# Optimization experiments

Hardware: AMD Instinct MI355X
Metric: run time of the kernel (lower is better)

Reference implementation:

```python
import jax, jax.numpy as jnp
import numpy as np

B, S, D_IN, D_OUT, RANK, HBS, ABS = 4, 2048, 4096, 4096, 32, 128, 16


def _hadamard(n: int) -> np.ndarray:
    H = np.array([[1.0]], dtype=np.float64)
    while H.shape[0] < n:
        H = np.block([[H, H], [H, -H]])
    return (H / np.sqrt(n)).astype(np.float32)


def setup_inputs() -> dict:
    key = jax.random.key(0)
    ks = jax.random.split(key, 6)
    x = jax.random.normal(ks[0], (B, S, D_IN), dtype=jnp.float32)
    # random +/-1 sign vector (matches torch.randint(0,2)*2-1)
    S_in = (jax.random.randint(ks[1], (D_IN,), 0, 2) * 2 - 1).astype(jnp.float32)
    H_block = jnp.asarray(_hadamard(HBS))  # orthonormal block Hadamard
    w_quantized = jax.random.normal(ks[2], (D_OUT, D_IN), dtype=jnp.float32) * 0.02
    lora_a = jax.random.normal(ks[3], (RANK, D_IN), dtype=jnp.float32) * 0.01
    lora_b = jax.random.normal(ks[4], (D_OUT, RANK), dtype=jnp.float32) * 0.01
    bias = jax.random.normal(ks[5], (D_OUT,), dtype=jnp.float32) * 0.01
    return {"x": x, "S_in": S_in, "H_block": H_block, "w_quantized": w_quantized,
            "lora_a": lora_a, "lora_b": lora_b, "bias": bias}


def _quantize_nvfp4(x, block_size=ABS):
    # per-block (size 16) NVFP4 fake-quant; numel here is divisible by block_size
    levels = jnp.array([0.0, 0.5, 1.0, 1.5, 2.0, 3.0, 4.0, 6.0], dtype=x.dtype)
    shape = x.shape
    xf = x.reshape(-1, block_size)
    amax = jnp.maximum(jnp.max(jnp.abs(xf), axis=-1, keepdims=True), 1e-12)
    scale = amax / 6.0
    x_norm = jnp.abs(xf) / scale
    idx = jnp.argmin(jnp.abs(x_norm[..., None] - levels), axis=-1)  # snap to grid
    xq = jnp.sign(xf) * levels[idx] * scale
    return xq.reshape(shape)


def _hadamard_rotate(x, S_in, H_block):
    # sign flip then block-diagonal Hadamard on the last dim
    shape = x.shape
    x_s = x * S_in
    x3 = x_s.reshape(*shape[:-1], shape[-1] // HBS, HBS)
    return (x3 @ H_block).reshape(shape)


def reference(x, S_in, H_block, w_quantized, lora_a, lora_b, bias):
    x_rot = _hadamard_rotate(x, S_in, H_block)          # [B,S,D_IN]
    x_q = _quantize_nvfp4(x_rot)                        # NVFP4 fake-quant activations
    out = jnp.einsum('bsd,od->bso', x_q, w_quantized)   # main GEMM
    # LoRA correction on the (unquantized) rotated activations
    out = out + jnp.einsum('bsr,or->bso', jnp.einsum('bsd,rd->bsr', x_rot, lora_a), lora_b)
    out = out + bias
    return out
```

## Files before the change

### kernel.cpp

```cpp
#include <hip/hip_runtime.h>

#define M_ROWS 8192
#define DIN    4096
#define DOUT   4096
#define RANK   32
#define KAUG   4128

typedef __attribute__((ext_vector_type(8))) short short8;
typedef __attribute__((ext_vector_type(4))) float floatx4;

__device__ __forceinline__ unsigned short f2bf(float f) {
    unsigned int u = __float_as_uint(f);
    unsigned int r = (u + 0x7FFFu + ((u >> 16) & 1u)) >> 16;
    return (unsigned short)r;
}

__global__ __launch_bounds__(256) void rot_quant_kernel(
    const float* __restrict__ x, const float* __restrict__ sgn,
    const float* __restrict__ lora_a, unsigned short* __restrict__ xaug)
{
    __shared__ float xs[4096];
    __shared__ float tred[RANK][9];

    const int row = blockIdx.x;
    const int t = threadIdx.x;
    const float* xr = x + (size_t)row * DIN;

    #pragma unroll
    for (int it = 0; it < 4; ++it) {
        int i4 = it * 256 + t;
        float4 v = ((const float4*)xr)[i4];
        float4 s = ((const float4*)sgn)[i4];
        v.x *= s.x; v.y *= s.y; v.z *= s.z; v.w *= s.w;
        ((float4*)xs)[i4] = v;
    }
    __syncthreads();

    for (int h = 1; h < 128; h <<= 1) {
        #pragma unroll
        for (int p = t; p < 2048; p += 256) {
            int i = ((p & ~(h - 1)) << 1) | (p & (h - 1));
            float a = xs[i], b = xs[i + h];
            xs[i] = a + b;
            xs[i + h] = a - b;
        }
        __syncthreads();
    }

    const float inv = 0.08838834764831845f;

    {
        float v[16];
        float amax = 0.f;
        #pragma unroll
        for (int j = 0; j < 16; ++j) {
            v[j] = xs[16 * t + j] * inv;
            amax = fmaxf(amax, fabsf(v[j]));
        }
        amax = fmaxf(amax, 1e-12f);
        float scale = amax / 6.0f;
        unsigned int pk[8];
        #pragma unroll
        for (int j = 0; j < 8; ++j) {
            unsigned short q2[2];
            #pragma unroll
            for (int e = 0; e < 2; ++e) {
                float vv = v[2 * j + e];
                float an = fabsf(vv) / scale;
                float lev = 0.0f;
                lev = an > 0.25f ? 0.5f : lev;
                lev = an > 0.75f ? 1.0f : lev;
                lev = an > 1.25f ? 1.5f : lev;
                lev = an > 1.75f ? 2.0f : lev;
                lev = an > 2.5f  ? 3.0f : lev;
                lev = an > 3.5f  ? 4.0f : lev;
                lev = an > 5.0f  ? 6.0f : lev;
                q2[e] = f2bf(copysignf(lev * scale, vv));
            }
            pk[j] = (unsigned int)q2[0] | ((unsigned int)q2[1] << 16);
        }
        unsigned short* orow = xaug + (size_t)row * KAUG + 16 * t;
        uint4 pk0 = make_uint4(pk[0], pk[1], pk[2], pk[3]);
        uint4 pk1 = make_uint4(pk[4], pk[5], pk[6], pk[7]);
        ((uint4*)orow)[0] = pk0;
        ((uint4*)orow)[1] = pk1;
    }

    {
        int r = t >> 3, oct = t & 7;
        const float* ar = lora_a + (size_t)r * DIN;
        float sum = 0.f;
        for (int d0 = oct * 4; d0 < DIN; d0 += 32) {
            float4 a4 = *(const float4*)(ar + d0);
            float4 x4 = *(const float4*)(xs + d0);
            sum += a4.x * x4.x + a4.y * x4.y + a4.z * x4.z + a4.w * x4.w;
        }
        tred[r][oct] = sum;
    }
    __syncthreads();
    if (t < RANK) {
        float s = 0.f;
        #pragma unroll
        for (int k = 0; k < 8; ++k) s += tred[t][k];
        s *= inv;
        xaug[(size_t)row * KAUG + DIN + t] = f2bf(s);
    }
}

__global__ __launch_bounds__(256) void cast_w_kernel(
    const float* __restrict__ w, const float* __restrict__ lora_b,
    unsigned short* __restrict__ waug)
{
    const int n = blockIdx.x;
    unsigned short* wr = waug + (size_t)n * KAUG;
    const float* wsrc = w + (size_t)n * DIN;
    #pragma unroll
    for (int j = threadIdx.x; j < DIN; j += 256) wr[j] = f2bf(wsrc[j]);
    if (threadIdx.x < RANK)
        wr[DIN + threadIdx.x] = f2bf(lora_b[(size_t)n * RANK + threadIdx.x]);
}

__global__ __launch_bounds__(256) void gemm_kernel(
    const unsigned short* __restrict__ A,
    const unsigned short* __restrict__ Bm,
    const float* __restrict__ bias,
    float* __restrict__ C)
{
    __shared__ unsigned short As[128 * 32];
    __shared__ unsigned short Bs[128 * 32];

    const int nt = blockIdx.x & 31;
    const int mt = blockIdx.x >> 5;
    const int m0 = mt * 128, n0 = nt * 128;
    const int t = threadIdx.x;
    const int wave = t >> 6, lane = t & 63;
    const int wm = wave & 1, wn = wave >> 1;
    const int lm = lane & 15, lq = lane >> 4;

    floatx4 acc[4][4] = {};

    for (int kk = 0; kk < KAUG; kk += 32) {
        __syncthreads();
        {
            const int c0 = wave * 2;
            const int r_ = (c0 << 4) + (lane >> 2);
            const int colb = (lane & 3) << 3;
            const unsigned short* ga = A + (size_t)(m0 + r_) * KAUG + kk + colb;
            __builtin_amdgcn_global_load_lds(
                (const __attribute__((address_space(1))) void*)ga,
                (__attribute__((address_space(3))) void*)(As + (c0 << 9)), 16, 0, 0);
            __builtin_amdgcn_global_load_lds(
                (const __attribute__((address_space(1))) void*)(ga + (size_t)16 * KAUG),
                (__attribute__((address_space(3))) void*)(As + ((c0 + 1) << 9)), 16, 0, 0);
            const unsigned short* gb = Bm + (size_t)(n0 + r_) * KAUG + kk + colb;
            __builtin_amdgcn_global_load_lds(
                (const __attribute__((address_space(1))) void*)gb,
                (__attribute__((address_space(3))) void*)(Bs + (c0 << 9)), 16, 0, 0);
            __builtin_amdgcn_global_load_lds(
                (const __attribute__((address_space(1))) void*)(gb + (size_t)16 * KAUG),
                (__attribute__((address_space(3))) void*)(Bs + ((c0 + 1) << 9)), 16, 0, 0);
        }
        __syncthreads();

        short8 af[4], bfr[4];
        #pragma unroll
        for (int mi = 0; mi < 4; ++mi)
            af[mi] = *(const short8*)&As[(wm * 64 + mi * 16 + lm) * 32 + lq * 8];
        #pragma unroll
        for (int ni = 0; ni < 4; ++ni)
            bfr[ni] = *(const short8*)&Bs[(wn * 64 + ni * 16 + lm) * 32 + lq * 8];
        #pragma unroll
        for (int mi = 0; mi < 4; ++mi)
            #pragma unroll
            for (int ni = 0; ni < 4; ++ni)
                acc[mi][ni] = __builtin_amdgcn_mfma_f32_16x16x32_bf16(
                    af[mi], bfr[ni], acc[mi][ni], 0, 0, 0);
    }

    float bv[4];
    #pragma unroll
    for (int ni = 0; ni < 4; ++ni)
        bv[ni] = bias[n0 + wn * 64 + ni * 16 + lm];
    #pragma unroll
    for (int mi = 0; mi < 4; ++mi) {
        #pragma unroll
        for (int ni = 0; ni < 4; ++ni) {
            const int col = n0 + wn * 64 + ni * 16 + lm;
            #pragma unroll
            for (int r = 0; r < 4; ++r) {
                const int rowm = m0 + wm * 64 + mi * 16 + lq * 4 + r;
                C[(size_t)rowm * DOUT + col] = acc[mi][ni][r] + bv[ni];
            }
        }
    }
}

extern "C" void kernel_launch(void* const* d_in, const int* in_sizes, int n_in,
                              void* d_out, int out_size, void* d_ws, size_t ws_size,
                              hipStream_t stream) {
    const float* x      = (const float*)d_in[0];
    const float* sgn    = (const float*)d_in[1];
    const float* w      = (const float*)d_in[3];
    const float* lora_a = (const float*)d_in[4];
    const float* lora_b = (const float*)d_in[5];
    const float* bias   = (const float*)d_in[6];
    float* out = (float*)d_out;

    unsigned short* xaug = (unsigned short*)d_ws;
    unsigned short* waug = xaug + (size_t)M_ROWS * KAUG;

    rot_quant_kernel<<<M_ROWS, 256, 0, stream>>>(x, sgn, lora_a, xaug);
    cast_w_kernel<<<DOUT, 256, 0, stream>>>(w, lora_b, waug);
    gemm_kernel<<<(M_ROWS / 128) * (DOUT / 128), 256, 0, stream>>>(xaug, waug, bias, out);
}
```

Baseline: 781.9 us.

## Swizzle GEMM LDS tiles, batch rows in rot_quant, vectorize weight cast

Applies an XOR swizzle to the LDS column placement of the A/B tiles in the GEMM so that the MFMA fragment reads hit fewer LDS bank conflicts. The rotate/quantize kernel now handles four rows per block, reusing each lora_a load across four rows, and replaces the LDS reduction with wavefront shuffles. The weight cast uses float4 loads and packed 16-byte stores. The 64KB LDS per block in rot_quant may reduce its occupancy.

```diff
diff --git a/kernel.cpp b/kernel.cpp
--- a/kernel.cpp
+++ b/kernel.cpp
@@ -5,6 +5,7 @@
 #define DOUT   4096
 #define RANK   32
 #define KAUG   4128
+#define RROWS  4
 
 typedef __attribute__((ext_vector_type(8))) short short8;
 typedef __attribute__((ext_vector_type(4))) float floatx4;
@@ -19,42 +20,45 @@
     const float* __restrict__ x, const float* __restrict__ sgn,
     const float* __restrict__ lora_a, unsigned short* __restrict__ xaug)
 {
-    __shared__ float xs[4096];
-    __shared__ float tred[RANK][9];
-
-    const int row = blockIdx.x;
+    __shared__ float xs[RROWS][4096];
+
+    const int row0 = blockIdx.x * RROWS;
     const int t = threadIdx.x;
-    const float* xr = x + (size_t)row * DIN;
 
     #pragma unroll
     for (int it = 0; it < 4; ++it) {
         int i4 = it * 256 + t;
-        float4 v = ((const float4*)xr)[i4];
         float4 s = ((const float4*)sgn)[i4];
-        v.x *= s.x; v.y *= s.y; v.z *= s.z; v.w *= s.w;
-        ((float4*)xs)[i4] = v;
+        #pragma unroll
+        for (int r = 0; r < RROWS; ++r) {
+            float4 v = ((const float4*)(x + (size_t)(row0 + r) * DIN))[i4];
+            v.x *= s.x; v.y *= s.y; v.z *= s.z; v.w *= s.w;
+            ((float4*)xs[r])[i4] = v;
+        }
     }
     __syncthreads();
 
     for (int h = 1; h < 128; h <<= 1) {
         #pragma unroll
-        for (int p = t; p < 2048; p += 256) {
-            int i = ((p & ~(h - 1)) << 1) | (p & (h - 1));
-            float a = xs[i], b = xs[i + h];
-            xs[i] = a + b;
-            xs[i + h] = a - b;
+        for (int p = t; p < 2048 * RROWS; p += 256) {
+            int r = p >> 11, q = p & 2047;
+            int i = ((q & ~(h - 1)) << 1) | (q & (h - 1));
+            float a = xs[r][i], b = xs[r][i + h];
+            xs[r][i] = a + b;
+            xs[r][i + h] = a - b;
         }
         __syncthreads();
     }
 
     const float inv = 0.08838834764831845f;
 
-    {
+    #pragma unroll
+    for (int r = 0; r < RROWS; ++r) {
         float v[16];
         float amax = 0.f;
         #pragma unroll
         for (int j = 0; j < 16; ++j) {
-            v[j] = xs[16 * t + j] * inv;
+            v[j] = xs[r][16 * t + j] * inv;
             amax = fmaxf(amax, fabsf(v[j]));
         }
         amax = fmaxf(amax, 1e-12f);
@@ -79,31 +83,39 @@
             }
             pk[j] = (unsigned int)q2[0] | ((unsigned int)q2[1] << 16);
         }
-        unsigned short* orow = xaug + (size_t)row * KAUG + 16 * t;
-        uint4 pk0 = make_uint4(pk[0], pk[1], pk[2], pk[3]);
-        uint4 pk1 = make_uint4(pk[4], pk[5], pk[6], pk[7]);
-        ((uint4*)orow)[0] = pk0;
-        ((uint4*)orow)[1] = pk1;
+        unsigned short* orow = xaug + (size_t)(row0 + r) * KAUG + 16 * t;
+        ((uint4*)orow)[0] = make_uint4(pk[0], pk[1], pk[2], pk[3]);
+        ((uint4*)orow)[1] = make_uint4(pk[4], pk[5], pk[6], pk[7]);
     }
 
     {
-        int r = t >> 3, oct = t & 7;
-        const float* ar = lora_a + (size_t)r * DIN;
-        float sum = 0.f;
+        int rk = t >> 3, oct = t & 7;
+        const float* ar = lora_a + (size_t)rk * DIN;
+        float s0 = 0.f, s1 = 0.f, s2 = 0.f, s3 = 0.f;
         for (int d0 = oct * 4; d0 < DIN; d0 += 32) {
             float4 a4 = *(const float4*)(ar + d0);
-            float4 x4 = *(const float4*)(xs + d0);
-            sum += a4.x * x4.x + a4.y * x4.y + a4.z * x4.z + a4.w * x4.w;
-        }
-        tred[r][oct] = sum;
-    }
-    __syncthreads();
-    if (t < RANK) {
-        float s = 0.f;
-        #pragma unroll
-        for (int k = 0; k < 8; ++k) s += tred[t][k];
-        s *= inv;
-        xaug[(size_t)row * KAUG + DIN + t] = f2bf(s);
+            float4 x0 = *(const float4*)(&xs[0][d0]);
+            float4 x1 = *(const float4*)(&xs[1][d0]);
+            float4 x2 = *(const float4*)(&xs[2][d0]);
+            float4 x3 = *(const float4*)(&xs[3][d0]);
+            s0 += a4.x * x0.x + a4.y * x0.y + a4.z * x0.z + a4.w * x0.w;
+            s1 += a4.x * x1.x + a4.y * x1.y + a4.z * x1.z + a4.w * x1.w;
+            s2 += a4.x * x2.x + a4.y * x2.y + a4.z * x2.z + a4.w * x2.w;
+            s3 += a4.x * x3.x + a4.y * x3.y + a4.z * x3.z + a4.w * x3.w;
+        }
+        #pragma unroll
+        for (int m = 1; m < 8; m <<= 1) {
+            s0 += __shfl_xor(s0, m, 64);
+            s1 += __shfl_xor(s1, m, 64);
+            s2 += __shfl_xor(s2, m, 64);
+            s3 += __shfl_xor(s3, m, 64);
+        }
+        if (oct == 0) {
+            xaug[(size_t)(row0 + 0) * KAUG + DIN + rk] = f2bf(s0 * inv);
+            xaug[(size_t)(row0 + 1) * KAUG + DIN + rk] = f2bf(s1 * inv);
+            xaug[(size_t)(row0 + 2) * KAUG + DIN + rk] = f2bf(s2 * inv);
+            xaug[(size_t)(row0 + 3) * KAUG + DIN + rk] = f2bf(s3 * inv);
+        }
     }
 }
 
@@ -112,12 +124,26 @@
     unsigned short* __restrict__ waug)
 {
     const int n = blockIdx.x;
+    const int t = threadIdx.x;
     unsigned short* wr = waug + (size_t)n * KAUG;
-    const float* wsrc = w + (size_t)n * DIN;
-    #pragma unroll
-    for (int j = threadIdx.x; j < DIN; j += 256) wr[j] = f2bf(wsrc[j]);
-    if (threadIdx.x < RANK)
-        wr[DIN + threadIdx.x] = f2bf(lora_b[(size_t)n * RANK + threadIdx.x]);
+    const float* wsrc = w + (size_t)n * DIN + 16 * t;
+    float4 f0 = ((const float4*)wsrc)[0];
+    float4 f1 = ((const float4*)wsrc)[1];
+    float4 f2 = ((const float4*)wsrc)[2];
+    float4 f3 = ((const float4*)wsrc)[3];
+    uint4 p0, p1;
+    p0.x = (unsigned int)f2bf(f0.x) | ((unsigned int)f2bf(f0.y) << 16);
+    p0.y = (unsigned int)f2bf(f0.z) | ((unsigned int)f2bf(f0.w) << 16);
+    p0.z = (unsigned int)f2bf(f1.x) | ((unsigned int)f2bf(f1.y) << 16);
+    p0.w = (unsigned int)f2bf(f1.z) | ((unsigned int)f2bf(f1.w) << 16);
+    p1.x = (unsigned int)f2bf(f2.x) | ((unsigned int)f2bf(f2.y) << 16);
+    p1.y = (unsigned int)f2bf(f2.z) | ((unsigned int)f2bf(f2.w) << 16);
+    p1.z = (unsigned int)f2bf(f3.x) | ((unsigned int)f2bf(f3.y) << 16);
+    p1.w = (unsigned int)f2bf(f3.z) | ((unsigned int)f2bf(f3.w) << 16);
+    ((uint4*)(wr + 16 * t))[0] = p0;
+    ((uint4*)(wr + 16 * t))[1] = p1;
+    if (t < RANK)
+        wr[DIN + t] = f2bf(lora_b[(size_t)n * RANK + t]);
 }
 
 __global__ __launch_bounds__(256) void gemm_kernel(
@@ -136,15 +162,17 @@
     const int wave = t >> 6, lane = t & 63;
     const int wm = wave & 1, wn = wave >> 1;
     const int lm = lane & 15, lq = lane >> 4;
+    const int sw = ((lm >> 1) & 3);
 
     floatx4 acc[4][4] = {};
+
+    const int c0 = wave * 2;
+    const int r_ = (c0 << 4) + (lane >> 2);
+    const int colb = ((lane & 3) ^ ((lane >> 3) & 3)) << 3;
 
     for (int kk = 0; kk < KAUG; kk += 32) {
         __syncthreads();
         {
-            const int c0 = wave * 2;
-            const int r_ = (c0 << 4) + (lane >> 2);
-            const int colb = (lane & 3) << 3;
             const unsigned short* ga = A + (size_t)(m0 + r_) * KAUG + kk + colb;
             __builtin_amdgcn_global_load_lds(
                 (const __attribute__((address_space(1))) void*)ga,
@@ -165,10 +193,10 @@
         short8 af[4], bfr[4];
         #pragma unroll
         for (int mi = 0; mi < 4; ++mi)
-            af[mi] = *(const short8*)&As[(wm * 64 + mi * 16 + lm) * 32 + lq * 8];
+            af[mi] = *(const short8*)&As[(wm * 64 + mi * 16 + lm) * 32 + ((lq ^ sw) << 3)];
         #pragma unroll
         for (int ni = 0; ni < 4; ++ni)
-            bfr[ni] = *(const short8*)&Bs[(wn * 64 + ni * 16 + lm) * 32 + lq * 8];
+            bfr[ni] = *(const short8*)&Bs[(wn * 64 + ni * 16 + lm) * 32 + ((lq ^ sw) << 3)];
         #pragma unroll
         for (int mi = 0; mi < 4; ++mi)
             #pragma unroll
@@ -209,7 +237,7 @@
     unsigned short* xaug = (unsigned short*)d_ws;
     unsigned short* waug = xaug + (size_t)M_ROWS * KAUG;
 
-    rot_quant_kernel<<<M_ROWS, 256, 0, stream>>>(x, sgn, lora_a, xaug);
+    rot_quant_kernel<<<M_ROWS / RROWS, 256, 0, stream>>>(x, sgn, lora_a, xaug);
     cast_w_kernel<<<DOUT, 256, 0, stream>>>(w, lora_b, waug);
     gemm_kernel<<<(M_ROWS / 128) * (DOUT / 128), 256, 0, stream>>>(xaug, waug, bias, out);
 }
```

After: 842.8 us. +7.8%, slower.
